# Performance work log

Measured on AMD Instinct MI355X. Metric: run time of the kernel, lower is better.

The kernel has to match this reference:

```python
import jax, jax.numpy as jnp
import numpy as np

H = 16  # n_heads


def _ln(x, g, b, eps=1e-5):
    m = x.mean(-1, keepdims=True)
    v = ((x - m) ** 2).mean(-1, keepdims=True)
    return (x - m) / jnp.sqrt(v + eps) * g + b


def setup_inputs() -> dict:
    key = jax.random.key(0)
    ks = jax.random.split(key, 10)
    b, lq, d, dff, L = 2, 1024, 1024, 4096, 4
    s = 0.02
    return {
        "x": jax.random.normal(ks[0], (b, lq, d), jnp.float32),
        "memory_bank": jax.random.normal(ks[1], (L, b, lq, d), jnp.float32),
        "attn_mask": jax.random.bernoulli(ks[2], 0.3, (b, lq, lq)),
        "ln1_g": jnp.ones((d,), jnp.float32),
        "ln1_b": jnp.zeros((d,), jnp.float32),
        "Wq": jax.random.normal(ks[3], (d, d), jnp.float32) * s,
        "Wk": jax.random.normal(ks[4], (d, d), jnp.float32) * s,
        "Wv": jax.random.normal(ks[5], (d, d), jnp.float32) * s,
        "Wo": jax.random.normal(ks[6], (d, d), jnp.float32) * s,
        "ln2_g": jnp.ones((d,), jnp.float32),
        "ln2_b": jnp.zeros((d,), jnp.float32),
        "W1": jax.random.normal(ks[7], (d, dff), jnp.float32) * s,
        "b1": jnp.zeros((dff,), jnp.float32),
        "W2": jax.random.normal(ks[8], (dff, d), jnp.float32) * s,
        "b2": jnp.zeros((d,), jnp.float32),
    }


def reference(x, memory_bank, attn_mask, ln1_g, ln1_b, Wq, Wk, Wv, Wo,
              ln2_g, ln2_b, W1, b1, W2, b2):
    # x: [b, lq, d]; memory_bank: [L, b, lk, d]; attn_mask: [b, lq, lk] bool (True = masked)
    b, lq, d = x.shape
    dh = d // H
    # preprocess_attn: LayerNorm (eval mode -> dropouts are identity)
    q = _ln(x, ln1_g, ln1_b)
    # grow memory bank with current normalized input
    mem = jnp.concatenate([memory_bank, q[None]], axis=0)  # [L+1, b, lk, d]
    L, _, lk, _ = mem.shape
    # projections (bias-free); key/value projected per layer then flattened over (L, lk)
    pq = (q @ Wq).reshape(b, lq, H, dh).transpose(0, 2, 1, 3) * (dh ** -0.5)  # [b,h,lq,dh]
    pk = (mem @ Wk).transpose(1, 0, 2, 3).reshape(b, L * lk, H, dh).transpose(0, 2, 1, 3)
    pv = (mem @ Wv).transpose(1, 0, 2, 3).reshape(b, L * lk, H, dh).transpose(0, 2, 1, 3)
    scores = jnp.einsum('bhqd,bhkd->bhqk', pq, pk)           # [b,h,lq,L*lk]
    scores = scores.reshape(b, H, lq, L, lk)
    scores = jnp.where(attn_mask[:, None, :, None, :], -jnp.inf, scores)
    attn = jax.nn.softmax(scores.reshape(b, H, lq, L * lk), axis=-1)
    ctx = jnp.einsum('bhqk,bhkd->bhqd', attn, pv)            # [b,h,lq,dh]
    ctx = ctx.transpose(0, 2, 1, 3).reshape(b, lq, d)
    attn_out = ctx @ Wo
    # postprocess_attn: residual add
    x2 = x + attn_out
    # FFN: LayerNorm -> Linear -> ReLU -> Linear -> residual
    f = _ln(x2, ln2_g, ln2_b)
    f = jax.nn.relu(f @ W1 + b1) @ W2 + b2
    out = x2 + f
    return (out, mem)
```

## Files before the change

kernel.cpp:

```cpp
#include <hip/hip_runtime.h>
#include <hip/hip_bf16.h>

typedef __attribute__((ext_vector_type(8))) __bf16 bf16x8;
typedef __attribute__((ext_vector_type(4))) __bf16 bf16x4;
typedef __attribute__((ext_vector_type(4))) float f32x4;
typedef __attribute__((ext_vector_type(16))) float f32x16;

#define MFMA16(a, b, c) __builtin_amdgcn_mfma_f32_16x16x32_bf16((a), (b), (c), 0, 0, 0)
#define MFMA32(a, b, c) __builtin_amdgcn_mfma_f32_32x32x16_bf16((a), (b), (c), 0, 0, 0)
#define LOG2E 1.4426950408889634f

static __device__ __forceinline__ float exp2_fast(float x) {
    float r; asm("v_exp_f32 %0, %1" : "=v"(r) : "v"(x)); return r;
}

__device__ __forceinline__ void gll16(const void* g, void* l) {
    __builtin_amdgcn_global_load_lds((const __attribute__((address_space(1))) void*)g,
                                     (__attribute__((address_space(3))) void*)l,
                                     16, 0, 0);
}

__global__ __launch_bounds__(256) void prep_kernel(const float* __restrict__ bank,
                                                   float* __restrict__ mem_out,
                                                   __bf16* __restrict__ membf,
                                                   const float* __restrict__ x,
                                                   const float* __restrict__ g,
                                                   const float* __restrict__ bta,
                                                   float* __restrict__ q_out,
                                                   __bf16* __restrict__ qbf,
                                                   const float* __restrict__ Wq,
                                                   const float* __restrict__ Wk,
                                                   const float* __restrict__ Wv,
                                                   __bf16* __restrict__ Wq_t,
                                                   __bf16* __restrict__ Wkv_t,
                                                   const unsigned char* __restrict__ mask,
                                                   unsigned int* __restrict__ mbits) {
    __shared__ float rs[4], rs2[4];
    __shared__ float tile[32][33];
    int blk = blockIdx.x;
    if (blk < 2048) {
        int i = blk * 256 + threadIdx.x;
        const float4* i4 = (const float4*)bank;
        float4* o4 = (float4*)mem_out;
        for (; i < 2097152; i += 2048 * 256) {
            float4 v = i4[i];
            o4[i] = v;
            if (membf) {
                bf16x4 ob = {(__bf16)v.x, (__bf16)v.y, (__bf16)v.z, (__bf16)v.w};
                ((bf16x4*)membf)[i] = ob;
            }
        }
    } else if (blk < 4096) {
        int row = blk - 2048;
        const float4 v = ((const float4*)(x + (size_t)row * 1024))[threadIdx.x];
        float s = v.x + v.y + v.z + v.w;
        float s2 = v.x * v.x + v.y * v.y + v.z * v.z + v.w * v.w;
#pragma unroll
        for (int off = 1; off < 64; off <<= 1) {
            s += __shfl_xor(s, off);
            s2 += __shfl_xor(s2, off);
        }
        int wv = threadIdx.x >> 6;
        if ((threadIdx.x & 63) == 0) { rs[wv] = s; rs2[wv] = s2; }
        __syncthreads();
        s = rs[0] + rs[1] + rs[2] + rs[3];
        s2 = rs2[0] + rs2[1] + rs2[2] + rs2[3];
        float mean = s * (1.0f / 1024.0f);
        float var = s2 * (1.0f / 1024.0f) - mean * mean;
        float rstd = rsqrtf(var + 1e-5f);
        float4 gg = ((const float4*)g)[threadIdx.x];
        float4 bb = ((const float4*)bta)[threadIdx.x];
        float4 o;
        o.x = (v.x - mean) * rstd * gg.x + bb.x;
        o.y = (v.y - mean) * rstd * gg.y + bb.y;
        o.z = (v.z - mean) * rstd * gg.z + bb.z;
        o.w = (v.w - mean) * rstd * gg.w + bb.w;
        ((float4*)(q_out + (size_t)row * 1024))[threadIdx.x] = o;
        if (qbf) {
            bf16x4 ob = {(__bf16)o.x, (__bf16)o.y, (__bf16)o.z, (__bf16)o.w};
            ((bf16x4*)(qbf + (size_t)row * 1024))[threadIdx.x] = ob;
        }
    } else if (blk < 7168) {
        int w = blk - 4096;
        int sel = w >> 10, within = w & 1023;
        const float* in = (sel == 0) ? Wq : ((sel == 1) ? Wk : Wv);
        __bf16* out = (sel == 0) ? Wq_t : (Wkv_t + (size_t)(sel - 1) * 1048576);
        int k0 = (within >> 5) * 32, n0 = (within & 31) * 32;
        int tx = threadIdx.x & 31, ty = threadIdx.x >> 5;
#pragma unroll
        for (int i = 0; i < 4; i++)
            tile[ty + i * 8][tx] = in[(size_t)(k0 + ty + i * 8) * 1024 + n0 + tx];
        __syncthreads();
#pragma unroll
        for (int i = 0; i < 4; i++)
            out[(size_t)(n0 + ty + i * 8) * 1024 + k0 + tx] = (__bf16)tile[tx][ty + i * 8];
    } else if (mbits) {
        int row = blk - 7168;
        const unsigned char* mrow = mask + (size_t)row * 1024;
        int wv = threadIdx.x >> 6, l = threadIdx.x & 63;
        unsigned long long* dst = (unsigned long long*)(mbits + (size_t)row * 32);
#pragma unroll
        for (int i = 0; i < 4; i++) {
            int key = i * 256 + wv * 64 + l;
            unsigned long long bal = __ballot(mrow[key] != 0);
            if (l == 0) dst[i * 4 + wv] = bal;
        }
    }
}

__global__ __launch_bounds__(256) void vtr_kernel(const __bf16* __restrict__ PV,
                                                  __bf16* __restrict__ PVt) {
    __shared__ __bf16 tile[64][72];
    int w = blockIdx.x;
    int bh = w / 80, kt = w % 80;
    int b = bh >> 4, h = bh & 15;
    int lidx = kt >> 4, i0 = (kt & 15) * 64;
    int kg0 = lidx * 2048 + b * 1024 + i0;
    int r = threadIdx.x >> 2, c16 = (threadIdx.x & 3) * 16;
    const __bf16* src = PV + (size_t)(kg0 + r) * 1024 + h * 64 + c16;
    *(bf16x8*)&tile[r][c16] = *(const bf16x8*)src;
    *(bf16x8*)&tile[r][c16 + 8] = *(const bf16x8*)(src + 8);
    __syncthreads();
    int dh = threadIdx.x >> 2, k0 = (threadIdx.x & 3) * 16;
    bf16x8 o0, o1;
#pragma unroll
    for (int j = 0; j < 8; j++) {
        o0[j] = tile[k0 + j][dh];
        o1[j] = tile[k0 + 8 + j][dh];
    }
    __bf16* dst = PVt + (size_t)(bh * 64 + dh) * 5120 + kt * 64 + k0;
    *(bf16x8*)dst = o0;
    *(bf16x8*)(dst + 8) = o1;
}

__global__ __launch_bounds__(256) void ln_kernel(const float* __restrict__ x,
                                                 const float* __restrict__ g,
                                                 const float* __restrict__ bta,
                                                 __bf16* __restrict__ outb) {
    int row = blockIdx.x;
    const float4 v = ((const float4*)(x + (size_t)row * 1024))[threadIdx.x];
    float s = v.x + v.y + v.z + v.w;
    float s2 = v.x * v.x + v.y * v.y + v.z * v.z + v.w * v.w;
#pragma unroll
    for (int off = 1; off < 64; off <<= 1) {
        s += __shfl_xor(s, off);
        s2 += __shfl_xor(s2, off);
    }
    __shared__ float rs[4], rs2[4];
    int wv = threadIdx.x >> 6;
    if ((threadIdx.x & 63) == 0) { rs[wv] = s; rs2[wv] = s2; }
    __syncthreads();
    s = rs[0] + rs[1] + rs[2] + rs[3];
    s2 = rs2[0] + rs2[1] + rs2[2] + rs2[3];
    float mean = s * (1.0f / 1024.0f);
    float var = s2 * (1.0f / 1024.0f) - mean * mean;
    float rstd = rsqrtf(var + 1e-5f);
    float4 gg = ((const float4*)g)[threadIdx.x];
    float4 bb = ((const float4*)bta)[threadIdx.x];
    bf16x4 ob;
    ob[0] = (__bf16)((v.x - mean) * rstd * gg.x + bb.x);
    ob[1] = (__bf16)((v.y - mean) * rstd * gg.y + bb.y);
    ob[2] = (__bf16)((v.z - mean) * rstd * gg.z + bb.z);
    ob[3] = (__bf16)((v.w - mean) * rstd * gg.w + bb.w);
    ((bf16x4*)(outb + (size_t)row * 1024))[threadIdx.x] = ob;
}

__global__ __launch_bounds__(256) void comb_ln2(const float* __restrict__ pc0,
                                                const float* __restrict__ pc1,
                                                const float* __restrict__ pc2,
                                                const float* __restrict__ pc3,
                                                const float* __restrict__ x,
                                                const float* __restrict__ g,
                                                const float* __restrict__ bta,
                                                float* __restrict__ x2,
                                                __bf16* __restrict__ fln) {
    int row = blockIdx.x;
    int idx = row * 256 + threadIdx.x;
    float4 a = ((const float4*)pc0)[idx];
    float4 b = ((const float4*)pc1)[idx];
    float4 c = ((const float4*)pc2)[idx];
    float4 d = ((const float4*)pc3)[idx];
    float4 r = ((const float4*)x)[idx];
    float4 v;
    v.x = (a.x + b.x) + (c.x + d.x) + r.x;
    v.y = (a.y + b.y) + (c.y + d.y) + r.y;
    v.z = (a.z + b.z) + (c.z + d.z) + r.z;
    v.w = (a.w + b.w) + (c.w + d.w) + r.w;
    ((float4*)x2)[idx] = v;
    float s = v.x + v.y + v.z + v.w;
    float s2 = v.x * v.x + v.y * v.y + v.z * v.z + v.w * v.w;
#pragma unroll
    for (int off = 1; off < 64; off <<= 1) {
        s += __shfl_xor(s, off);
        s2 += __shfl_xor(s2, off);
    }
    __shared__ float rs[4], rs2[4];
    int wv = threadIdx.x >> 6;
    if ((threadIdx.x & 63) == 0) { rs[wv] = s; rs2[wv] = s2; }
    __syncthreads();
    s = rs[0] + rs[1] + rs[2] + rs[3];
    s2 = rs2[0] + rs2[1] + rs2[2] + rs2[3];
    float mean = s * (1.0f / 1024.0f);
    float var = s2 * (1.0f / 1024.0f) - mean * mean;
    float rstd = rsqrtf(var + 1e-5f);
    float4 gg = ((const float4*)g)[threadIdx.x];
    float4 bb = ((const float4*)bta)[threadIdx.x];
    bf16x4 ob;
    ob[0] = (__bf16)((v.x - mean) * rstd * gg.x + bb.x);
    ob[1] = (__bf16)((v.y - mean) * rstd * gg.y + bb.y);
    ob[2] = (__bf16)((v.z - mean) * rstd * gg.z + bb.z);
    ob[3] = (__bf16)((v.w - mean) * rstd * gg.w + bb.w);
    ((bf16x4*)(fln + (size_t)row * 1024))[threadIdx.x] = ob;
}

__device__ __forceinline__ void tr_body(const float* __restrict__ in, __bf16* __restrict__ out,
                                        int K, int N, int k0, int n0) {
    __shared__ float tile[32][33];
    int tx = threadIdx.x & 31, ty = threadIdx.x >> 5;
#pragma unroll
    for (int i = 0; i < 4; i++)
        tile[ty + i * 8][tx] = in[(size_t)(k0 + ty + i * 8) * N + n0 + tx];
    __syncthreads();
#pragma unroll
    for (int i = 0; i < 4; i++)
        out[(size_t)(n0 + ty + i * 8) * K + k0 + tx] = (__bf16)tile[tx][ty + i * 8];
}

__global__ __launch_bounds__(256) void tr_late(const float* __restrict__ Wo,
                                               const float* __restrict__ W1,
                                               const float* __restrict__ W2,
                                               __bf16* __restrict__ Wo_t,
                                               __bf16* __restrict__ W1_t,
                                               __bf16* __restrict__ W2_t) {
    int w = blockIdx.x;
    const float* in;
    __bf16* out;
    int K, N, k0, n0;
    if (w < 1024) {
        in = Wo; out = Wo_t; K = 1024; N = 1024; n0 = (w & 31) * 32; k0 = (w >> 5) * 32;
    } else if (w < 5120) {
        int v = w - 1024;
        in = W1; out = W1_t; K = 1024; N = 4096; n0 = (v & 127) * 32; k0 = (v >> 7) * 32;
    } else {
        int v = w - 5120;
        in = W2; out = W2_t; K = 4096; N = 1024; n0 = (v & 31) * 32; k0 = (v >> 5) * 32;
    }
    tr_body(in, out, K, N, k0, n0);
}

template <int EPI, bool ABF16>
__device__ __forceinline__ void gemm_core(const void* __restrict__ Av,
                                          const __bf16* __restrict__ Bt,
                                          void* __restrict__ Cout,
                                          const float* __restrict__ bias,
                                          const float* __restrict__ res,
                                          int N, int lda, int ldb, int klen,
                                          float scale, int bm, int bn) {
    constexpr int LDA = ABF16 ? 32 : 40;
    __shared__ __bf16 As[128 * LDA];
    __shared__ __bf16 Bs[128 * 32];

    int t = threadIdx.x;
    int lane = t & 63, wave = t >> 6;
    int wm = (wave >> 1) * 64, wn = (wave & 1) * 64;
    int l16 = lane & 15, l4 = lane >> 4;

    f32x4 acc[4][4];
#pragma unroll
    for (int m = 0; m < 4; m++)
#pragma unroll
        for (int n = 0; n < 4; n++) acc[m][n] = (f32x4){0.f, 0.f, 0.f, 0.f};

    int srow = t >> 2;
    int scol = (t & 3) * 8;
    int ar = t >> 1, ak = (t & 1) * 16;
    const __bf16* Ab = (const __bf16*)Av;
    const float* Af = (const float*)Av;

    for (int k0 = 0; k0 < klen; k0 += 32) {
        gll16(Bt + (size_t)(bn + srow) * ldb + (k0 + scol), &Bs[wave * 512]);
        gll16(Bt + (size_t)(bn + 64 + srow) * ldb + (k0 + scol), &Bs[2048 + wave * 512]);
        if constexpr (ABF16) {
            gll16(Ab + (size_t)(bm + srow) * lda + (k0 + scol), &As[wave * 512]);
            gll16(Ab + (size_t)(bm + 64 + srow) * lda + (k0 + scol), &As[2048 + wave * 512]);
        } else {
            const float* ap = Af + (size_t)(bm + ar) * lda + k0 + ak;
            float4 f0 = ((const float4*)ap)[0];
            float4 f1 = ((const float4*)ap)[1];
            float4 f2 = ((const float4*)ap)[2];
            float4 f3 = ((const float4*)ap)[3];
            float ta[16] = {f0.x, f0.y, f0.z, f0.w, f1.x, f1.y, f1.z, f1.w,
                            f2.x, f2.y, f2.z, f2.w, f3.x, f3.y, f3.z, f3.w};
            bf16x8 v0, v1;
#pragma unroll
            for (int j = 0; j < 8; j++) { v0[j] = (__bf16)ta[j]; v1[j] = (__bf16)ta[j + 8]; }
            *(bf16x8*)&As[ar * 40 + ak] = v0;
            *(bf16x8*)&As[ar * 40 + ak + 8] = v1;
        }
        __syncthreads();

        bf16x8 af[4], bfr[4];
#pragma unroll
        for (int m = 0; m < 4; m++) af[m] = *(const bf16x8*)&As[(wm + m * 16 + l16) * LDA + l4 * 8];
#pragma unroll
        for (int n = 0; n < 4; n++) bfr[n] = *(const bf16x8*)&Bs[(wn + n * 16 + l16) * 32 + l4 * 8];
#pragma unroll
        for (int m = 0; m < 4; m++)
#pragma unroll
            for (int n = 0; n < 4; n++) acc[m][n] = MFMA16(af[m], bfr[n], acc[m][n]);
        __syncthreads();
    }

#pragma unroll
    for (int m = 0; m < 4; m++) {
#pragma unroll
        for (int r = 0; r < 4; r++) {
            int row = bm + wm + m * 16 + l4 * 4 + r;
#pragma unroll
            for (int n = 0; n < 4; n++) {
                int col = bn + wn + n * 16 + l16;
                float c = acc[m][n][r];
                size_t idx = (size_t)row * N + col;
                if (EPI == 0) {
                    ((__bf16*)Cout)[idx] = (__bf16)(c * scale);
                } else if (EPI == 1) {
                    ((float*)Cout)[idx] = c + res[idx];
                } else if (EPI == 2) {
                    ((__bf16*)Cout)[idx] = (__bf16)fmaxf(c + bias[col], 0.0f);
                } else if (EPI == 3) {
                    ((float*)Cout)[idx] = c + bias[col] + res[idx];
                } else {
                    ((float*)Cout)[idx] = c;
                }
            }
        }
    }
}

template <int EPI, bool ABF16>
__global__ __launch_bounds__(256) void gemm_bt(const void* __restrict__ Av,
                                               const __bf16* __restrict__ Bt,
                                               void* __restrict__ Cout,
                                               const float* __restrict__ bias,
                                               const float* __restrict__ res,
                                               int N, int K, float scale, int nbx) {
    int q = gridDim.x >> 3;
    int swz = (blockIdx.x & 7) * q + (blockIdx.x >> 3);
    int bn = (swz % nbx) * 128;
    int bm = (swz / nbx) * 128;
    gemm_core<EPI, ABF16>(Av, Bt, Cout, bias, res, N, K, K, K, scale, bm, bn);
}

template <bool ABF16>
__global__ __launch_bounds__(256) void gemm_proj(const void* __restrict__ Akv,
                                                 const __bf16* __restrict__ Wkv_t,
                                                 __bf16* __restrict__ PK,
                                                 __bf16* __restrict__ PV,
                                                 const void* __restrict__ Aq,
                                                 const __bf16* __restrict__ Wq_t,
                                                 __bf16* __restrict__ Pq) {
    int q = gridDim.x >> 3;
    int swz = (blockIdx.x & 7) * q + (blockIdx.x >> 3);
    if (swz < 1280) {
        int bn = (swz & 15) * 128, bm = (swz >> 4) * 128;
        __bf16* C = (bn < 1024) ? PK : PV;
        int bnl = bn & 1023;
        const __bf16* Bt = Wkv_t + ((size_t)(bn & 1024) << 10);
        gemm_core<0, ABF16>(Akv, Bt, C, nullptr, nullptr, 1024, 1024, 1024, 1024, 1.0f, bm, bnl);
    } else {
        int p = swz - 1280;
        int bn = (p & 7) * 128, bm = (p >> 3) * 128;
        gemm_core<0, ABF16>(Aq, Wq_t, Pq, nullptr, nullptr, 1024, 1024, 1024, 1024,
                            0.125f * LOG2E, bm, bn);
    }
}

__global__ __launch_bounds__(256) void gemm_w2(const __bf16* __restrict__ h1,
                                               const __bf16* __restrict__ W2_t,
                                               float* __restrict__ pc0,
                                               float* __restrict__ pc1,
                                               float* __restrict__ pc2,
                                               float* __restrict__ pc3) {
    int q = gridDim.x >> 3;
    int swz = (blockIdx.x & 7) * q + (blockIdx.x >> 3);
    int quarter = swz >> 7;
    int p = swz & 127;
    int bn = (p & 7) * 128, bm = (p >> 3) * 128;
    int koff = quarter * 1024;
    float* pc = (quarter == 0) ? pc0 : (quarter == 1) ? pc1 : (quarter == 2) ? pc2 : pc3;
    gemm_core<4, true>(h1 + koff, W2_t + koff, pc, nullptr, nullptr,
                       1024, 4096, 4096, 1024, 1.0f, bm, bn);
}

__global__ __launch_bounds__(256) void gemm_wo(const __bf16* __restrict__ ctx,
                                               const __bf16* __restrict__ Wo_t,
                                               float* __restrict__ pc0,
                                               float* __restrict__ pc1,
                                               float* __restrict__ pc2,
                                               float* __restrict__ pc3) {
    int q = gridDim.x >> 3;
    int swz = (blockIdx.x & 7) * q + (blockIdx.x >> 3);
    int quarter = swz >> 7;
    int p = swz & 127;
    int bn = (p & 7) * 128, bm = (p >> 3) * 128;
    int koff = quarter * 256;
    float* pc = (quarter == 0) ? pc0 : (quarter == 1) ? pc1 : (quarter == 2) ? pc2 : pc3;
    gemm_core<4, true>(ctx + koff, Wo_t + koff, pc, nullptr, nullptr,
                       1024, 1024, 1024, 256, 1.0f, bm, bn);
}

__global__ __launch_bounds__(256) void comb_kernel(const float* __restrict__ pc0,
                                                   const float* __restrict__ pc1,
                                                   const float* __restrict__ pc2,
                                                   const float* __restrict__ pc3,
                                                   const float* __restrict__ bias,
                                                   const float* __restrict__ res,
                                                   float* __restrict__ out) {
    int i = blockIdx.x * 256 + threadIdx.x;
    float4 a = ((const float4*)pc0)[i];
    float4 b = ((const float4*)pc1)[i];
    float4 c = ((const float4*)pc2)[i];
    float4 d = ((const float4*)pc3)[i];
    float4 r = ((const float4*)res)[i];
    float4 o;
    o.x = (a.x + b.x) + (c.x + d.x) + r.x;
    o.y = (a.y + b.y) + (c.y + d.y) + r.y;
    o.z = (a.z + b.z) + (c.z + d.z) + r.z;
    o.w = (a.w + b.w) + (c.w + d.w) + r.w;
    if (bias) {
        float4 bb = ((const float4*)bias)[i & 255];
        o.x += bb.x; o.y += bb.y; o.z += bb.z; o.w += bb.w;
    }
    ((float4*)out)[i] = o;
}

__device__ __forceinline__ void softmax_p(const f32x16& s0, const f32x16& s1,
                                          unsigned int mka, unsigned int mkb,
                                          int hi, float& lsum, bf16x8* pf) {
    unsigned int ow[8][2];
#pragma unroll
    for (int g = 0; g < 4; g++) {
        bf16x4 p0, p1;
#pragma unroll
        for (int m = 0; m < 4; m++) {
            float e = exp2_fast(s0[g * 4 + m]);
            e = ((mka >> (g * 8 + hi * 4 + m)) & 1u) ? 0.0f : e;
            lsum += e;
            p0[m] = (__bf16)e;
            float e2 = exp2_fast(s1[g * 4 + m]);
            e2 = ((mkb >> (g * 8 + hi * 4 + m)) & 1u) ? 0.0f : e2;
            lsum += e2;
            p1[m] = (__bf16)e2;
        }
        ow[g][0] = ((unsigned int*)&p0)[0];
        ow[g][1] = ((unsigned int*)&p0)[1];
        ow[4 + g][0] = ((unsigned int*)&p1)[0];
        ow[4 + g][1] = ((unsigned int*)&p1)[1];
    }
#pragma unroll
    for (int ks = 0; ks < 4; ks++) {
        unsigned int a0 = ow[2 * ks][0], b0 = ow[2 * ks + 1][0];
        unsigned int a1 = ow[2 * ks][1], b1 = ow[2 * ks + 1][1];
        asm volatile("v_permlane32_swap_b32 %0, %1" : "+v"(a0), "+v"(b0));
        asm volatile("v_permlane32_swap_b32 %0, %1" : "+v"(a1), "+v"(b1));
        unsigned int* pp = (unsigned int*)&pf[ks];
        pp[0] = a0; pp[1] = a1; pp[2] = b0; pp[3] = b1;
    }
}

#define NCHP 20
__global__ __launch_bounds__(256, 2) void attn_tr(const __bf16* __restrict__ Pq,
                                                  const __bf16* __restrict__ PK,
                                                  const __bf16* __restrict__ PVt,
                                                  const unsigned int* __restrict__ mbits,
                                                  __bf16* __restrict__ pacc,
                                                  float* __restrict__ pl,
                                                  const float* __restrict__ Wo,
                                                  const float* __restrict__ W1,
                                                  const float* __restrict__ W2,
                                                  __bf16* __restrict__ Wo_t,
                                                  __bf16* __restrict__ W1_t,
                                                  __bf16* __restrict__ W2_t) {
    __shared__ char smem[32768];
    int blk = blockIdx.x;
    if (blk >= 1024) {
        float (*tile)[33] = (float(*)[33])smem;
        int w = blk - 1024;
        const float* in;
        __bf16* out;
        int K, N, k0, n0;
        if (w < 1024) {
            in = Wo; out = Wo_t; K = 1024; N = 1024; n0 = (w & 31) * 32; k0 = (w >> 5) * 32;
        } else if (w < 5120) {
            int v = w - 1024;
            in = W1; out = W1_t; K = 1024; N = 4096; n0 = (v & 127) * 32; k0 = (v >> 7) * 32;
        } else {
            int v = w - 5120;
            in = W2; out = W2_t; K = 4096; N = 1024; n0 = (v & 31) * 32; k0 = (v >> 5) * 32;
        }
        int tx = threadIdx.x & 31, ty = threadIdx.x >> 5;
#pragma unroll
        for (int i = 0; i < 4; i++)
            tile[ty + i * 8][tx] = in[(size_t)(k0 + ty + i * 8) * N + n0 + tx];
        __syncthreads();
#pragma unroll
        for (int i = 0; i < 4; i++)
            out[(size_t)(n0 + ty + i * 8) * K + k0 + tx] = (__bf16)tile[tx][ty + i * 8];
        return;
    }

    __bf16 (*KB)[64][64] = (__bf16(*)[64][64])smem;
    __bf16 (*VB)[64][64] = (__bf16(*)[64][64])(smem + 16384);

    int bh = blk & 31;
    int qb = (blk >> 5) & 7;
    int rng = blk >> 8;
    int b = bh >> 4, h = bh & 15;
    int wave = threadIdx.x >> 6, lane = threadIdx.x & 63;
    int l32 = lane & 31, hi = lane >> 5;
    int q0 = qb * 128 + wave * 32;

    bf16x8 qf[4];
    {
        const __bf16* pqrow = Pq + (size_t)(b * 1024 + q0 + l32) * 1024 + h * 64 + hi * 8;
#pragma unroll
        for (int ds = 0; ds < 4; ds++) qf[ds] = *(const bf16x8*)(pqrow + ds * 16);
    }

    f32x16 acc0, acc1;
#pragma unroll
    for (int i = 0; i < 16; i++) { acc0[i] = 0.f; acc1[i] = 0.f; }
    float lsum = 0.0f;

    const unsigned int* mrow0 = mbits + (size_t)(b * 1024 + q0 + l32) * 32;

    int kgbase = rng * 1280;

    int idxA = wave * 8 + (lane >> 3);
    int idxB = (wave + 4) * 8 + (lane >> 3);
    int GA = (idxA ^ (idxA >> 3)) & 7;
    int GB = (idxB ^ (idxB >> 3)) & 7;
    int swA = (((lane & 7) ^ GA) << 4);
    int swB = (((lane & 7) ^ GB) << 4);
    size_t koffA = (size_t)idxA * 2048 + swA;
    size_t koffB = (size_t)idxB * 2048 + swB;
    size_t voffA = (size_t)idxA * 10240 + swA;
    size_t voffB = (size_t)idxB * 10240 + swB;

    int kmod = kgbase & 1023;
    const char* pkc = (const char*)PK + ((size_t)((kgbase >> 10) * 2048 + b * 1024 + kmod)) * 2048
                      + (size_t)h * 128;
    const char* pvc = (const char*)PVt + (size_t)(bh * 64) * 10240 + (size_t)kgbase * 2;

#define STAGE(BUF)                                            \
    do {                                                      \
        gll16(pkc + koffA, &KB[BUF][wave * 8][0]);            \
        gll16(pkc + koffB, &KB[BUF][(wave + 4) * 8][0]);      \
        gll16(pvc + voffA, &VB[BUF][wave * 8][0]);            \
        gll16(pvc + voffB, &VB[BUF][(wave + 4) * 8][0]);      \
    } while (0)
#define ADV()                                                          \
    do {                                                               \
        int st = (kmod + 64 >= 1024) ? (64 + 1024) : 64;               \
        kmod = (kmod + 64) & 1023;                                     \
        pkc += (size_t)st * 2048;                                      \
        pvc += 128;                                                    \
    } while (0)

    STAGE(0);
    ADV();
    int kd0 = (kgbase & 1023) >> 5;
    unsigned int mk0a = mrow0[kd0], mk0b = mrow0[kd0 + 1];

    int Gr0 = (l32 ^ (l32 >> 3)) & 7;
    int r1v = 32 + l32;
    int Gr1 = (r1v ^ (r1v >> 3)) & 7;

    for (int t = 0; t < NCHP; t++) {
        int buf = t & 1;
        __syncthreads();
        if (t + 1 < NCHP) {
            STAGE(buf ^ 1);
            ADV();
        }
        unsigned int nk0a = 0, nk0b = 0;
        if (t + 1 < NCHP) {
            int kdn = ((kgbase + (t + 1) * 64) & 1023) >> 5;
            nk0a = mrow0[kdn]; nk0b = mrow0[kdn + 1];
        }

        const __bf16* KsF = &KB[buf][0][0];
        const __bf16* VtF = &VB[buf][0][0];

        f32x16 s0, s1;
#pragma unroll
        for (int i = 0; i < 16; i++) { s0[i] = 0.f; s1[i] = 0.f; }
        __builtin_amdgcn_s_setprio(1);
#pragma unroll
        for (int ds = 0; ds < 4; ds++) {
            bf16x8 ka0 = *(const bf16x8*)&KsF[l32 * 64 + (((ds * 2 + hi) ^ Gr0) << 3)];
            bf16x8 ka1 = *(const bf16x8*)&KsF[r1v * 64 + (((ds * 2 + hi) ^ Gr1) << 3)];
            s0 = MFMA32(ka0, qf[ds], s0);
            s1 = MFMA32(ka1, qf[ds], s1);
        }
        __builtin_amdgcn_s_setprio(0);

        bf16x8 pf0[4];
        softmax_p(s0, s1, mk0a, mk0b, hi, lsum, pf0);

        mk0a = nk0a; mk0b = nk0b;

        __builtin_amdgcn_s_setprio(1);
#pragma unroll
        for (int ks = 0; ks < 4; ks++) {
            bf16x8 vf0 = *(const bf16x8*)&VtF[l32 * 64 + (((ks * 2 + hi) ^ Gr0) << 3)];
            bf16x8 vf1 = *(const bf16x8*)&VtF[r1v * 64 + (((ks * 2 + hi) ^ Gr1) << 3)];
            acc0 = MFMA32(vf0, pf0[ks], acc0);
            acc1 = MFMA32(vf1, pf0[ks], acc1);
        }
        __builtin_amdgcn_s_setprio(0);
    }
#undef STAGE
#undef ADV

    lsum += __shfl_xor(lsum, 32);

    size_t oblk = ((size_t)(bh * 8 + qb) * 4 + rng);
    __bf16* pa = pacc + oblk * 8192 + (size_t)(wave * 32 + l32) * 64;
#pragma unroll
    for (int g = 0; g < 4; g++) {
        bf16x4 o0, o1;
#pragma unroll
        for (int m = 0; m < 4; m++) {
            o0[m] = (__bf16)acc0[g * 4 + m];
            o1[m] = (__bf16)acc1[g * 4 + m];
        }
        *(bf16x4*)&pa[g * 8 + hi * 4] = o0;
        *(bf16x4*)&pa[32 + g * 8 + hi * 4] = o1;
    }
    if (hi == 0) pl[oblk * 128 + wave * 32 + l32] = lsum;
}

__global__ __launch_bounds__(256) void attn_comb(const __bf16* __restrict__ pacc,
                                                 const float* __restrict__ pl,
                                                 __bf16* __restrict__ ctx) {
    int bh = blockIdx.x, qb = blockIdx.y;
    int b = bh >> 4, h = bh & 15;
    int q = threadIdx.x >> 1, dhalf = (threadIdx.x & 1) * 32;
    float acc[32];
#pragma unroll
    for (int j = 0; j < 32; j++) acc[j] = 0.0f;
    float l = 0.0f;
    size_t blk0 = ((size_t)(bh * 8 + qb)) * 4;
#pragma unroll
    for (int rng = 0; rng < 4; rng++) {
        size_t base = (blk0 + rng) * 8192 + (size_t)q * 64 + dhalf;
#pragma unroll
        for (int v = 0; v < 4; v++) {
            bf16x8 a = *(const bf16x8*)&pacc[base + v * 8];
#pragma unroll
            for (int j = 0; j < 8; j++) acc[v * 8 + j] += (float)a[j];
        }
        l += pl[(blk0 + rng) * 128 + q];
    }
    float inv = 1.0f / l;
    __bf16* crow = ctx + ((size_t)(b * 1024 + qb * 128 + q) << 10) + h * 64 + dhalf;
#pragma unroll
    for (int v = 0; v < 4; v++) {
        bf16x8 o;
#pragma unroll
        for (int j = 0; j < 8; j++) o[j] = (__bf16)(acc[v * 8 + j] * inv);
        *(bf16x8*)&crow[v * 8] = o;
    }
}

#define KHALF 2560
#define CK 64
#define NCH 40
__global__ __launch_bounds__(512, 4) void attn_kernel(const __bf16* __restrict__ Pq,
                                                      const __bf16* __restrict__ PK,
                                                      const __bf16* __restrict__ PV,
                                                      const unsigned char* __restrict__ mask,
                                                      __bf16* __restrict__ ctx) {
    int bh = blockIdx.x;
    int b = bh >> 4, h = bh & 15;
    int wave = threadIdx.x >> 6, lane = threadIdx.x & 63;
    int grp = wave >> 2, wv = wave & 3;
    int l16 = lane & 15, l4 = lane >> 4;
    int q0 = blockIdx.y * 64 + wv * 16;

    __shared__ __bf16 Ks[2][64][72];
    __shared__ __bf16 Vt[2][64][72];
    __shared__ __bf16 Ps[8][16][72];

    const f32x4 fzero = {0.f, 0.f, 0.f, 0.f};

    bf16x8 qf[2];
    {
        const __bf16* pqrow = Pq + (size_t)(b * 1024 + q0 + l16) * 1024 + h * 64;
        qf[0] = *(const bf16x8*)(pqrow + l4 * 8);
        qf[1] = *(const bf16x8*)(pqrow + 32 + l4 * 8);
    }

    f32x4 accT[4];
#pragma unroll
    for (int n = 0; n < 4; n++) accT[n] = fzero;
    float lsum = 0.0f;

    const unsigned char* mrow_p = mask + (size_t)b * (1024u * 1024u) + (size_t)(q0 + l16) * 1024;

    int tl = threadIdx.x & 255;
    int skey = tl >> 2;
    int sd0 = (tl & 3) << 4;
    int kgbase = grp * KHALF;

    bf16x8 rk0, rk1, rv0, rv1;
    unsigned int mk[4], mkn[4];
    {
        int kg = kgbase + skey;
        int lidx = kg >> 10, i = kg & 1023;
        size_t off = (size_t)(lidx * 2048 + b * 1024 + i) * 1024 + h * 64 + sd0;
        rk0 = *(const bf16x8*)(PK + off);
        rk1 = *(const bf16x8*)(PK + off + 8);
        rv0 = *(const bf16x8*)(PV + off);
        rv1 = *(const bf16x8*)(PV + off + 8);
        int kloc = kgbase & 1023;
#pragma unroll
        for (int tile = 0; tile < 4; tile++)
            mk[tile] = *(const unsigned int*)(mrow_p + kloc + tile * 16 + l4 * 4);
    }

    for (int t = 0; t < NCH; t++) {
        *(bf16x8*)&Ks[grp][skey][sd0] = rk0;
        *(bf16x8*)&Ks[grp][skey][sd0 + 8] = rk1;
#pragma unroll
        for (int j = 0; j < 8; j++) {
            int row = sd0 + j;
            Vt[grp][row][skey ^ ((row >> 3) << 3)] = rv0[j];
            int row2 = sd0 + 8 + j;
            Vt[grp][row2][skey ^ ((row2 >> 3) << 3)] = rv1[j];
        }
        __syncthreads();

        if (t + 1 < NCH) {
            int kg = kgbase + (t + 1) * CK + skey;
            int lidx = kg >> 10, i = kg & 1023;
            size_t off = (size_t)(lidx * 2048 + b * 1024 + i) * 1024 + h * 64 + sd0;
            rk0 = *(const bf16x8*)(PK + off);
            rk1 = *(const bf16x8*)(PK + off + 8);
            rv0 = *(const bf16x8*)(PV + off);
            rv1 = *(const bf16x8*)(PV + off + 8);
            int kloc = (kgbase + (t + 1) * CK) & 1023;
#pragma unroll
            for (int tile = 0; tile < 4; tile++)
                mkn[tile] = *(const unsigned int*)(mrow_p + kloc + tile * 16 + l4 * 4);
        }

        f32x4 s[4];
        __builtin_amdgcn_s_setprio(1);
#pragma unroll
        for (int tile = 0; tile < 4; tile++) {
            bf16x8 ka = *(const bf16x8*)&Ks[grp][tile * 16 + l16][l4 * 8];
            bf16x8 kb = *(const bf16x8*)&Ks[grp][tile * 16 + l16][32 + l4 * 8];
            f32x4 sz = fzero;
            sz = MFMA16(ka, qf[0], sz);
            sz = MFMA16(kb, qf[1], sz);
            s[tile] = sz;
        }
        __builtin_amdgcn_s_setprio(0);

        float psum = 0.0f;
#pragma unroll
        for (int tile = 0; tile < 4; tile++) {
            bf16x4 pk_;
#pragma unroll
            for (int r = 0; r < 4; r++) {
                float e = exp2_fast(s[tile][r]);
                e = ((mk[tile] >> (r * 8)) & 255u) ? 0.0f : e;
                psum += e;
                pk_[r] = (__bf16)e;
            }
            *(bf16x4*)&Ps[wave][l16][tile * 16 + l4 * 4] = pk_;
        }
        lsum += psum;
#pragma unroll
        for (int tile = 0; tile < 4; tile++) mk[tile] = mkn[tile];

        __builtin_amdgcn_s_setprio(1);
#pragma unroll
        for (int kk = 0; kk < 2; kk++) {
            bf16x8 pf = *(const bf16x8*)&Ps[wave][l16][kk * 32 + l4 * 8];
#pragma unroll
            for (int n = 0; n < 4; n++) {
                int row = n * 16 + l16;
                int colblk = (kk * 32 + l4 * 8) ^ ((row >> 3) << 3);
                bf16x8 vf = *(const bf16x8*)&Vt[grp][row][colblk];
                accT[n] = MFMA16(vf, pf, accT[n]);
            }
        }
        __builtin_amdgcn_s_setprio(0);
        __syncthreads();
    }

    lsum += __shfl_xor(lsum, 16);
    lsum += __shfl_xor(lsum, 32);

    float* exAcc = (float*)&Ks[0][0][0];
    float* exL = (float*)&Vt[0][0][0];
    if (grp == 1) {
#pragma unroll
        for (int n = 0; n < 4; n++)
            *(f32x4*)&exAcc[(wv * 16 + l16) * 68 + n * 16 + l4 * 4] = accT[n];
        if (l4 == 0) exL[wv * 16 + l16] = lsum;
    }
    __syncthreads();
    if (grp == 0) {
        int qi = wv * 16 + l16;
        float inv = 1.0f / (lsum + exL[qi]);
        __bf16* crow = ctx + ((size_t)(b * 1024 + q0 + l16) << 10) + h * 64;
#pragma unroll
        for (int n = 0; n < 4; n++) {
            f32x4 a1 = *(const f32x4*)&exAcc[qi * 68 + n * 16 + l4 * 4];
            bf16x4 o;
#pragma unroll
            for (int r = 0; r < 4; r++) o[r] = (__bf16)((accT[n][r] + a1[r]) * inv);
            *(bf16x4*)&crow[n * 16 + l4 * 4] = o;
        }
    }
}

extern "C" void kernel_launch(void* const* d_in, const int* in_sizes, int n_in,
                              void* d_out, int out_size, void* d_ws, size_t ws_size,
                              hipStream_t stream) {
    const float* x = (const float*)d_in[0];
    const float* memory_bank = (const float*)d_in[1];
    const unsigned char* attn_mask = (const unsigned char*)d_in[2];
    const float* ln1_g = (const float*)d_in[3];
    const float* ln1_b = (const float*)d_in[4];
    const float* Wq = (const float*)d_in[5];
    const float* Wk = (const float*)d_in[6];
    const float* Wv = (const float*)d_in[7];
    const float* Wo = (const float*)d_in[8];
    const float* ln2_g = (const float*)d_in[9];
    const float* ln2_b = (const float*)d_in[10];
    const float* W1 = (const float*)d_in[11];
    const float* b1 = (const float*)d_in[12];
    const float* W2 = (const float*)d_in[13];
    const float* b2 = (const float*)d_in[14];

    float* out = (float*)d_out;
    float* mem_out = out + 2097152;
    float* q_out = mem_out + 4 * 2097152;

    char* ws = (char*)d_ws;
    bool big = ws_size >= (89ull << 20);

    __bf16* PK = (__bf16*)ws;
    __bf16* PV = (__bf16*)(ws + (20ull << 20));
    __bf16 *Pq, *Wq_t, *Wkv_t, *ctx, *membf = nullptr, *qbf = nullptr;
    __bf16 *Wo_t, *W1_t, *W2_t;
    __bf16* PVt = nullptr;
    __bf16* pacc = nullptr;
    float* plv = nullptr;
    unsigned int* mbits = nullptr;
    if (big) {
        membf = (__bf16*)(ws + (40ull << 20));
        qbf = membf + (size_t)8192 * 1024;
        Wq_t = (__bf16*)(ws + (60ull << 20));
        Wkv_t = (__bf16*)(ws + (62ull << 20));
        Pq = (__bf16*)(ws + (66ull << 20));
        mbits = (unsigned int*)(ws + (70ull << 20));
        Wo_t = (__bf16*)(ws + (71ull << 20));
        W1_t = (__bf16*)(ws + (73ull << 20));
        W2_t = (__bf16*)(ws + (81ull << 20));
        PVt = (__bf16*)(ws + (40ull << 20));
        pacc = (__bf16*)(ws + (20ull << 20));
        plv = (float*)(ws + (36ull << 20));
        ctx = (__bf16*)(ws + (60ull << 20));
    } else {
        Pq = (__bf16*)(ws + (40ull << 20));
        Wq_t = (__bf16*)(ws + (44ull << 20));
        Wkv_t = (__bf16*)(ws + (46ull << 20));
        ctx = (__bf16*)(ws + (44ull << 20));
        Wo_t = (__bf16*)ws;
        W1_t = (__bf16*)(ws + (2ull << 20));
        W2_t = (__bf16*)(ws + (10ull << 20));
    }
    float* x2 = (float*)(ws + (18ull << 20));
    __bf16* fln = (__bf16*)(ws + (26ull << 20));
    __bf16* h1 = (__bf16*)(ws + (30ull << 20));
    float* wo_pc0 = (float*)ws;
    float* wo_pc1 = (float*)(ws + (8ull << 20));
    float* wo_pc2 = (float*)(ws + (30ull << 20));
    float* wo_pc3 = (float*)(ws + (38ull << 20));
    float* pc0 = (float*)(ws + (46ull << 20));
    float* pc1 = (float*)(ws + (54ull << 20));
    float* pc2 = (float*)(ws + (62ull << 20));
    float* pc3 = (float*)(ws + (70ull << 20));

    prep_kernel<<<big ? 9216 : 7168, 256, 0, stream>>>(memory_bank, mem_out, membf, x,
                                                       ln1_g, ln1_b, q_out, qbf,
                                                       Wq, Wk, Wv, Wq_t, Wkv_t,
                                                       attn_mask, mbits);

    if (big)
        gemm_proj<true><<<1408, 256, 0, stream>>>(membf, Wkv_t, PK, PV, qbf, Wq_t, Pq);
    else
        gemm_proj<false><<<1408, 256, 0, stream>>>(mem_out, Wkv_t, PK, PV, q_out, Wq_t, Pq);

    if (big) {
        vtr_kernel<<<2560, 256, 0, stream>>>(PV, PVt);
        attn_tr<<<10240, 256, 0, stream>>>(Pq, PK, PVt, mbits, pacc, plv,
                                           Wo, W1, W2, Wo_t, W1_t, W2_t);
        attn_comb<<<dim3(32, 8), 256, 0, stream>>>(pacc, plv, ctx);
    } else {
        attn_kernel<<<dim3(32, 16), 512, 0, stream>>>(Pq, PK, PV, attn_mask, ctx);
        tr_late<<<9216, 256, 0, stream>>>(Wo, W1, W2, Wo_t, W1_t, W2_t);
    }

    if (big) {
        gemm_wo<<<512, 256, 0, stream>>>(ctx, Wo_t, wo_pc0, wo_pc1, wo_pc2, wo_pc3);
        comb_ln2<<<2048, 256, 0, stream>>>(wo_pc0, wo_pc1, wo_pc2, wo_pc3,
                                           x, ln2_g, ln2_b, x2, fln);
    } else {
        gemm_bt<1, true><<<128, 256, 0, stream>>>(ctx, Wo_t, x2, nullptr, x, 1024, 1024, 1.0f, 8);
        ln_kernel<<<2048, 256, 0, stream>>>(x2, ln2_g, ln2_b, fln);
    }
    gemm_bt<2, true><<<512, 256, 0, stream>>>(fln, W1_t, h1, b1, nullptr, 4096, 1024, 1.0f, 32);
    if (big) {
        gemm_w2<<<512, 256, 0, stream>>>(h1, W2_t, pc0, pc1, pc2, pc3);
        comb_kernel<<<2048, 256, 0, stream>>>(pc0, pc1, pc2, pc3, b2, x2, out);
    } else {
        gemm_bt<3, true><<<128, 256, 0, stream>>>(h1, W2_t, out, b2, x2, 1024, 4096, 1.0f, 8);
    }
}
```

Baseline: 244.2 us.

## Move memory-bank copy and mask bit-packing into the projection GEMM launch

On the big path, the fp32 copy of the memory bank to the output and the mask-to-bitmask packing move out of the prep kernel. They now run as extra trailing blocks of the projection GEMM kernel, whose grid grows to hold them. The aim is to shorten the prep kernel on the critical path and overlap these independent bandwidth-bound jobs with GEMM compute. The cost is that the extra blocks compete with GEMM blocks for CUs and bandwidth, and the GEMM swizzle now uses a hardcoded constant.

After: 245.2 us. About the same (+0.4%).

```diff
diff --git a/kernel.cpp b/kernel.cpp
--- a/kernel.cpp
+++ b/kernel.cpp
@@ -32,9 +32,7 @@
                                                    const float* __restrict__ Wk,
                                                    const float* __restrict__ Wv,
                                                    __bf16* __restrict__ Wq_t,
-                                                   __bf16* __restrict__ Wkv_t,
-                                                   const unsigned char* __restrict__ mask,
-                                                   unsigned int* __restrict__ mbits) {
+                                                   __bf16* __restrict__ Wkv_t) {
     __shared__ float rs[4], rs2[4];
     __shared__ float tile[32][33];
     int blk = blockIdx.x;
@@ -44,7 +42,7 @@
         float4* o4 = (float4*)mem_out;
         for (; i < 2097152; i += 2048 * 256) {
             float4 v = i4[i];
-            o4[i] = v;
+            if (mem_out) o4[i] = v;
             if (membf) {
                 bf16x4 ob = {(__bf16)v.x, (__bf16)v.y, (__bf16)v.z, (__bf16)v.w};
                 ((bf16x4*)membf)[i] = ob;
@@ -80,7 +78,7 @@
             bf16x4 ob = {(__bf16)o.x, (__bf16)o.y, (__bf16)o.z, (__bf16)o.w};
             ((bf16x4*)(qbf + (size_t)row * 1024))[threadIdx.x] = ob;
         }
-    } else if (blk < 7168) {
+    } else {
         int w = blk - 4096;
         int sel = w >> 10, within = w & 1023;
         const float* in = (sel == 0) ? Wq : ((sel == 1) ? Wk : Wv);
@@ -94,17 +92,6 @@
 #pragma unroll
         for (int i = 0; i < 4; i++)
             out[(size_t)(n0 + ty + i * 8) * 1024 + k0 + tx] = (__bf16)tile[tx][ty + i * 8];
-    } else if (mbits) {
-        int row = blk - 7168;
-        const unsigned char* mrow = mask + (size_t)row * 1024;
-        int wv = threadIdx.x >> 6, l = threadIdx.x & 63;
-        unsigned long long* dst = (unsigned long long*)(mbits + (size_t)row * 32);
-#pragma unroll
-        for (int i = 0; i < 4; i++) {
-            int key = i * 256 + wv * 64 + l;
-            unsigned long long bal = __ballot(mrow[key] != 0);
-            if (l == 0) dst[i * 4 + wv] = bal;
-        }
     }
 }
 
@@ -358,9 +345,34 @@
                                                  __bf16* __restrict__ PV,
                                                  const void* __restrict__ Aq,
                                                  const __bf16* __restrict__ Wq_t,
-                                                 __bf16* __restrict__ Pq) {
-    int q = gridDim.x >> 3;
-    int swz = (blockIdx.x & 7) * q + (blockIdx.x >> 3);
+                                                 __bf16* __restrict__ Pq,
+                                                 const float* __restrict__ bank,
+                                                 float* __restrict__ mem_out,
+                                                 const unsigned char* __restrict__ mask,
+                                                 unsigned int* __restrict__ mbits) {
+    int blk = blockIdx.x;
+    if (blk >= 1408) {
+        int w = blk - 1408;
+        if (w < 2048) {
+            int i = w * 256 + threadIdx.x;
+            const float4* i4 = (const float4*)bank;
+            float4* o4 = (float4*)mem_out;
+            for (; i < 2097152; i += 2048 * 256) o4[i] = i4[i];
+        } else {
+            int row = w - 2048;
+            const unsigned char* mrow = mask + (size_t)row * 1024;
+            int wv = threadIdx.x >> 6, l = threadIdx.x & 63;
+            unsigned long long* dst = (unsigned long long*)(mbits + (size_t)row * 32);
+#pragma unroll
+            for (int i = 0; i < 4; i++) {
+                int key = i * 256 + wv * 64 + l;
+                unsigned long long bal = __ballot(mrow[key] != 0);
+                if (l == 0) dst[i * 4 + wv] = bal;
+            }
+        }
+        return;
+    }
+    int swz = (blk & 7) * 176 + (blk >> 3);
     if (swz < 1280) {
         int bn = (swz & 15) * 128, bm = (swz >> 4) * 128;
         __bf16* C = (bn < 1024) ? PK : PV;
@@ -898,15 +910,16 @@
     float* pc2 = (float*)(ws + (62ull << 20));
     float* pc3 = (float*)(ws + (70ull << 20));
 
-    prep_kernel<<<big ? 9216 : 7168, 256, 0, stream>>>(memory_bank, mem_out, membf, x,
-                                                       ln1_g, ln1_b, q_out, qbf,
-                                                       Wq, Wk, Wv, Wq_t, Wkv_t,
-                                                       attn_mask, mbits);
+    prep_kernel<<<7168, 256, 0, stream>>>(memory_bank, big ? nullptr : mem_out, membf, x,
+                                          ln1_g, ln1_b, q_out, qbf,
+                                          Wq, Wk, Wv, Wq_t, Wkv_t);
 
     if (big)
-        gemm_proj<true><<<1408, 256, 0, stream>>>(membf, Wkv_t, PK, PV, qbf, Wq_t, Pq);
+        gemm_proj<true><<<5504, 256, 0, stream>>>(membf, Wkv_t, PK, PV, qbf, Wq_t, Pq,
+                                                  memory_bank, mem_out, attn_mask, mbits);
     else
-        gemm_proj<false><<<1408, 256, 0, stream>>>(mem_out, Wkv_t, PK, PV, q_out, Wq_t, Pq);
+        gemm_proj<false><<<1408, 256, 0, stream>>>(mem_out, Wkv_t, PK, PV, q_out, Wq_t, Pq,
+                                                   nullptr, nullptr, nullptr, nullptr);
 
     if (big) {
         vtr_kernel<<<2560, 256, 0, stream>>>(PV, PVt);
```
